# Kernel tuning notes

Hardware: AMD Instinct MI355X
Metric: run time of the kernel (lower is better)

The kernel has to match this reference:

```python
import jax, jax.numpy as jnp
import numpy as np

NUM_INTERVALS = 12
DOMAIN_MIN = -10.0
DOMAIN_MAX = 0.0


def _build_pla_coeffs(num_intervals=NUM_INTERVALS, dmin=DOMAIN_MIN, dmax=DOMAIN_MAX):
    """Least-squares linear fit of exp(x) on each interval (matches np.polyfit in source)."""
    xs = np.linspace(dmin, dmax, 1001)
    ys = np.exp(xs)
    edges = np.linspace(dmin, dmax, num_intervals + 1)
    ms, cs = [], []
    for i in range(num_intervals):
        mask = (xs >= edges[i]) & (xs <= edges[i + 1])
        m, c = np.polyfit(xs[mask], ys[mask], 1)
        ms.append(m)
        cs.append(c)
    # 'intervals' buffer in source stores only the LOWER edge of each interval (len = num_intervals)
    return (np.asarray(ms, np.float32), np.asarray(cs, np.float32), edges[:num_intervals].astype(np.float32))


def setup_inputs() -> dict:
    key = jax.random.key(0)
    scores = jax.random.normal(key, (8, 12, 512, 512), dtype=jnp.float32)
    m_np, c_np, a_np = _build_pla_coeffs()
    return {
        "scores": scores,
        "coeffs_m": jnp.asarray(m_np),
        "coeffs_c": jnp.asarray(c_np),
        "intervals": jnp.asarray(a_np),
    }


def reference(scores, coeffs_m, coeffs_c, intervals):
    # 1) stable shift by row max
    max_scores = jnp.max(scores, axis=-1, keepdims=True)
    shifted = scores - max_scores

    # 2) snap to Q32.26 fixed point
    fp_scale = 2.0 ** 26
    fx = jnp.clip(jnp.round(shifted * fp_scale), -(2.0 ** 31), 2.0 ** 31 - 1) / fp_scale

    # 3) piecewise-linear exp: bucket search against interval lower edges + coeff gather
    xc = jnp.clip(fx, DOMAIN_MIN, DOMAIN_MAX)
    # sum(x >= a_i) == searchsorted(a, x, side='right'); original clamps idx to len(intervals)-2
    idx = jnp.clip(jnp.searchsorted(intervals, xc, side="right") - 1, 0, intervals.shape[0] - 2)
    exps = coeffs_m[idx] * xc + coeffs_c[idx]

    # 4) normalize
    softmax_out = exps / (jnp.sum(exps, axis=-1, keepdims=True) + 1e-9)

    # 5) per-tensor symmetric INT8 fake-quant (STE form; same forward value)
    qmax = 127.0
    scale = jnp.maximum(jnp.max(jnp.abs(softmax_out)) / qmax, 1e-8)
    q = jnp.clip(jnp.round(softmax_out / scale), -qmax, qmax) * scale
    return softmax_out + jax.lax.stop_gradient(q - softmax_out)
```

## Files before the change

kernel.cpp:

```cpp
#include <hip/hip_runtime.h>

#define THREADS 256
#define WPB 4
#define ROW_LEN 512
#define NB 2048

typedef float f4 __attribute__((ext_vector_type(4)));
typedef char  c8 __attribute__((ext_vector_type(8)));

__device__ __forceinline__ float wave_reduce_max(float v) {
#pragma unroll
    for (int o = 32; o > 0; o >>= 1) v = fmaxf(v, __shfl_xor(v, o));
    return v;
}
__device__ __forceinline__ float wave_reduce_sum(float v) {
#pragma unroll
    for (int o = 32; o > 0; o >>= 1) v += __shfl_xor(v, o);
    return v;
}

__global__ __launch_bounds__(THREADS) void pla_pass0(
    const float* __restrict__ scores,
    const float* __restrict__ coeffs_m,
    const float* __restrict__ coeffs_c,
    const float* __restrict__ intervals,
    char* __restrict__ svq,
    float* __restrict__ rowg,
    float* __restrict__ slots,
    int nrows)
{
    __shared__ float2 s_mc[12];
    __shared__ float  s_a[13];
    __shared__ float  s_bm[WPB];

    const int tid = threadIdx.x;
    if (tid < 12) {
        s_mc[tid] = make_float2(coeffs_m[tid], coeffs_c[tid]);
        s_a[tid]  = intervals[tid];
    }
    if (tid == 12) s_a[12] = __builtin_inff();
    __syncthreads();

    const int wave = tid >> 6;
    const int lane = tid & 63;

    const float c10 = coeffs_c[10];
    const float k0  = 127.0f / c10;

    const int ngroups = (nrows + WPB - 1) / WPB;
    float bmax = 0.0f;

    for (int g = blockIdx.x; g < ngroups; g += NB) {
        const int row = g * WPB + wave;
        if (row >= nrows) continue;

        const float4* rp = reinterpret_cast<const float4*>(scores + (size_t)row * ROW_LEN);
        float4 v0 = rp[lane];
        float4 v1 = rp[lane + 64];
        float x[8] = {v0.x, v0.y, v0.z, v0.w, v1.x, v1.y, v1.z, v1.w};

        float mx = fmaxf(fmaxf(fmaxf(x[0], x[1]), fmaxf(x[2], x[3])),
                         fmaxf(fmaxf(x[4], x[5]), fmaxf(x[6], x[7])));
        mx = wave_reduce_max(mx);

        float e[8];
        float sum = 0.0f;
#pragma unroll
        for (int j = 0; j < 8; ++j) {
            float sh = x[j] - mx;
            float t = rintf(sh * 67108864.0f);
            float fx = t * 1.4901161193847656e-8f;
            float xc = fmaxf(fx, -10.0f);

            int gi = (int)((xc + 10.0f) * 1.2f);
            gi = min(max(gi, 0), 11);
            if (xc < s_a[gi])            gi -= 1;
            else if (xc >= s_a[gi + 1])  gi += 1;
            int idx = min(gi, 10);

            float2 p = s_mc[idx];
            float ev = p.x * xc + p.y;
            e[j] = ev;
            sum += ev;
        }
        sum = wave_reduce_sum(sum);
        const float inv = 1.0f / (sum + 1e-9f);

        c8 q;
#pragma unroll
        for (int j = 0; j < 8; ++j) q[j] = (char)(int)rintf(e[j] * k0);
        reinterpret_cast<c8*>(svq + (size_t)row * ROW_LEN)[lane] = q;

        if (lane == 0) {
            rowg[row] = c10 * inv * (1.0f / 127.0f);
            bmax = fmaxf(bmax, c10 * inv);
        }
    }

    if (lane == 0) s_bm[wave] = bmax;
    __syncthreads();
    if (tid == 0) {
        float bm = fmaxf(fmaxf(s_bm[0], s_bm[1]), fmaxf(s_bm[2], s_bm[3]));
        slots[blockIdx.x] = bm;
    }
}

__global__ __launch_bounds__(THREADS) void pla_pass1(
    const char* __restrict__ svq,
    const float* __restrict__ rowg,
    const float* __restrict__ slots,
    float* __restrict__ out,
    int nrows)
{
    __shared__ float s_red[WPB];
    const int tid  = threadIdx.x;
    const int wave = tid >> 6;
    const int lane = tid & 63;

    float m = 0.0f;
    for (int i = tid; i < NB; i += THREADS) m = fmaxf(m, slots[i]);
    m = wave_reduce_max(m);
    if (lane == 0) s_red[wave] = m;
    __syncthreads();
    const float am = fmaxf(fmaxf(s_red[0], s_red[1]), fmaxf(s_red[2], s_red[3]));

    const float scale  = fmaxf(am * (1.0f / 127.0f), 1e-8f);
    const float iscale = 1.0f / scale;

    const int ngroups = (nrows + WPB - 1) / WPB;
    for (int g = blockIdx.x; g < ngroups; g += NB) {
        const int row = g * WPB + wave;
        if (row >= nrows) continue;

        const float f = rowg[row] * iscale;
        c8 a = reinterpret_cast<const c8*>(svq + (size_t)row * ROW_LEN)[lane];

        float o[8];
#pragma unroll
        for (int j = 0; j < 8; ++j) {
            float q = fminf(fmaxf(rintf((float)a[j] * f), -127.0f), 127.0f);
            o[j] = q * scale;
        }
        f4* op = reinterpret_cast<f4*>(out + (size_t)row * ROW_LEN);
        f4 w0 = {o[0], o[1], o[2], o[3]};
        f4 w1 = {o[4], o[5], o[6], o[7]};
        __builtin_nontemporal_store(w0, op + lane);
        __builtin_nontemporal_store(w1, op + lane + 64);
    }
}

extern "C" void kernel_launch(void* const* d_in, const int* in_sizes, int n_in,
                              void* d_out, int out_size, void* d_ws, size_t ws_size,
                              hipStream_t stream) {
    const float* scores    = (const float*)d_in[0];
    const float* coeffs_m  = (const float*)d_in[1];
    const float* coeffs_c  = (const float*)d_in[2];
    const float* intervals = (const float*)d_in[3];
    float* out = (float*)d_out;

    const int nrows = in_sizes[0] / ROW_LEN;

    float* slots = (float*)d_ws;
    float* rowg  = (float*)((char*)d_ws + (128 << 10));
    char*  svq   = (char*)d_ws + (1 << 20);

    pla_pass0<<<NB, THREADS, 0, stream>>>(
        scores, coeffs_m, coeffs_c, intervals, svq, rowg, slots, nrows);
    pla_pass1<<<NB, THREADS, 0, stream>>>(svq, rowg, slots, out, nrows);
}
```

Baseline: 52.30 us.

## Fuse two passes into one persistent kernel with a grid-wide atomic barrier

Merges the two kernels into a single launch. Each block keeps its quantized rows and per-row factors in shared memory, publishes its block max, then spins on striped atomic counters until every block has arrived, reads the global max and writes the output. This removes the int8 workspace round-trip through global memory and the second kernel launch. In exchange it adds a memset, a spin-wait barrier that needs all 2048 blocks to be co-resident (launch bounds raised to 8 blocks per CU to allow that), and a fast path that only applies when the row count matches the fixed shape.

```diff
diff --git a/kernel.cpp b/kernel.cpp
--- a/kernel.cpp
+++ b/kernel.cpp
@@ -4,6 +4,10 @@
 #define WPB 4
 #define ROW_LEN 512
 #define NB 2048
+#define FTRIPS 6
+#define NCNT 64
+#define CSTRIDE 32
+#define AGENT __HIP_MEMORY_SCOPE_AGENT
 
 typedef float f4 __attribute__((ext_vector_type(4)));
 typedef char  c8 __attribute__((ext_vector_type(8)));
@@ -18,20 +22,44 @@
     for (int o = 32; o > 0; o >>= 1) v += __shfl_xor(v, o);
     return v;
 }
-
-__global__ __launch_bounds__(THREADS) void pla_pass0(
+__device__ __forceinline__ unsigned wave_reduce_sum_u(unsigned v) {
+#pragma unroll
+    for (int o = 32; o > 0; o >>= 1) v += __shfl_xor(v, o);
+    return v;
+}
+
+__device__ __forceinline__ float pla_eval(float xv, float mx,
+                                          const float* s_a, const float2* s_mc) {
+    float sh = xv - mx;
+    float t  = rintf(sh * 67108864.0f);
+    float fx = t * 1.4901161193847656e-8f;
+    float xc = fmaxf(fx, -10.0f);
+    int gi = (int)fmaf(xc, 1.2f, 12.0f);
+    gi = min(gi, 11);
+    if (xc < s_a[gi])            gi -= 1;
+    else if (xc >= s_a[gi + 1])  gi += 1;
+    int idx = min(gi, 10);
+    float2 p = s_mc[idx];
+    return fmaf(p.x, xc, p.y);
+}
+
+#define MAX8(x) fmaxf(fmaxf(fmaxf(x[0], x[1]), fmaxf(x[2], x[3])), \
+                      fmaxf(fmaxf(x[4], x[5]), fmaxf(x[6], x[7])))
+
+__global__ __launch_bounds__(THREADS, 8) void pla_fused(
     const float* __restrict__ scores,
     const float* __restrict__ coeffs_m,
     const float* __restrict__ coeffs_c,
     const float* __restrict__ intervals,
-    char* __restrict__ svq,
-    float* __restrict__ rowg,
-    float* __restrict__ slots,
-    int nrows)
+    float* __restrict__ bslots,
+    unsigned* __restrict__ counts,
+    float* __restrict__ out)
 {
     __shared__ float2 s_mc[12];
     __shared__ float  s_a[13];
     __shared__ float  s_bm[WPB];
+    __shared__ c8     s_q[WPB][FTRIPS][64];
+    __shared__ float  s_f[WPB][FTRIPS];
 
     const int tid = threadIdx.x;
     if (tid < 12) {
@@ -43,79 +71,152 @@
 
     const int wave = tid >> 6;
     const int lane = tid & 63;
-
     const float c10 = coeffs_c[10];
     const float k0  = 127.0f / c10;
 
+    float bmax = 0.0f;
+
+#pragma unroll
+    for (int t = 0; t < FTRIPS; ++t) {
+        const int row = (blockIdx.x + t * NB) * WPB + wave;
+        const f4* rp = reinterpret_cast<const f4*>(scores + (size_t)row * ROW_LEN);
+        f4 v0 = rp[lane];
+        f4 v1 = rp[lane + 64];
+        float x[8] = {v0.x, v0.y, v0.z, v0.w, v1.x, v1.y, v1.z, v1.w};
+
+        float mx = MAX8(x);
+        mx = wave_reduce_max(mx);
+
+        float sum = 0.0f;
+        c8 q;
+#pragma unroll
+        for (int j = 0; j < 8; ++j) {
+            float ev = pla_eval(x[j], mx, s_a, s_mc);
+            sum += ev;
+            q[j] = (char)(int)rintf(ev * k0);
+        }
+        s_q[wave][t][lane] = q;
+
+        sum = wave_reduce_sum(sum);
+        const float inv = 1.0f / (sum + 1e-9f);
+        if (lane == 0) {
+            s_f[wave][t] = c10 * inv * (1.0f / 127.0f);
+            bmax = fmaxf(bmax, c10 * inv);
+        }
+    }
+    if (lane == 0) s_bm[wave] = bmax;
+    __syncthreads();
+
+    if (tid == 0) {
+        float bm = fmaxf(fmaxf(s_bm[0], s_bm[1]), fmaxf(s_bm[2], s_bm[3]));
+        __hip_atomic_store(&bslots[blockIdx.x], bm, __ATOMIC_RELAXED, AGENT);
+        __hip_atomic_fetch_add(&counts[(blockIdx.x & (NCNT - 1)) * CSTRIDE],
+                               1u, __ATOMIC_RELEASE, AGENT);
+    }
+
+    if (tid < 64) {
+        unsigned total;
+        do {
+            __builtin_amdgcn_s_sleep(16);
+            unsigned c = __hip_atomic_load(&counts[tid * CSTRIDE],
+                                           __ATOMIC_RELAXED, AGENT);
+            total = wave_reduce_sum_u(c);
+        } while (total < (unsigned)NB);
+    }
+    __syncthreads();
+    __builtin_amdgcn_fence(__ATOMIC_ACQUIRE, "agent");
+
+    float m = 0.0f;
+    for (int i = tid; i < NB; i += THREADS)
+        m = fmaxf(m, __hip_atomic_load(&bslots[i], __ATOMIC_RELAXED, AGENT));
+    m = wave_reduce_max(m);
+    if (lane == 0) s_bm[wave] = m;
+    __syncthreads();
+    const float am = fmaxf(fmaxf(s_bm[0], s_bm[1]), fmaxf(s_bm[2], s_bm[3]));
+
+    const float scale  = fmaxf(am * (1.0f / 127.0f), 1e-8f);
+    const float iscale = 1.0f / scale;
+
+#pragma unroll
+    for (int t = 0; t < FTRIPS; ++t) {
+        const int row = (blockIdx.x + t * NB) * WPB + wave;
+        const float f = s_f[wave][t] * iscale;
+        c8 a = s_q[wave][t][lane];
+
+        float o[8];
+#pragma unroll
+        for (int j = 0; j < 8; ++j) {
+            float q = fminf(fmaxf(rintf((float)a[j] * f), -127.0f), 127.0f);
+            o[j] = q * scale;
+        }
+        f4* op = reinterpret_cast<f4*>(out + (size_t)row * ROW_LEN);
+        f4 w0 = {o[0], o[1], o[2], o[3]};
+        f4 w1 = {o[4], o[5], o[6], o[7]};
+        __builtin_nontemporal_store(w0, op + lane);
+        __builtin_nontemporal_store(w1, op + lane + 64);
+    }
+}
+
+__global__ __launch_bounds__(THREADS) void pla_pass0_gen(
+    const float* __restrict__ scores,
+    const float* __restrict__ coeffs_m,
+    const float* __restrict__ coeffs_c,
+    const float* __restrict__ intervals,
+    char* __restrict__ svq, float* __restrict__ rowg,
+    float* __restrict__ slots, int nrows)
+{
+    __shared__ float2 s_mc[12];
+    __shared__ float  s_a[13];
+    __shared__ float  s_bm[WPB];
+
+    const int tid = threadIdx.x;
+    if (tid < 12) {
+        s_mc[tid] = make_float2(coeffs_m[tid], coeffs_c[tid]);
+        s_a[tid]  = intervals[tid];
+    }
+    if (tid == 12) s_a[12] = __builtin_inff();
+    __syncthreads();
+
+    const int wave = tid >> 6, lane = tid & 63;
+    const float c10 = coeffs_c[10], k0 = 127.0f / c10;
+    float bmax = 0.0f;
+
     const int ngroups = (nrows + WPB - 1) / WPB;
-    float bmax = 0.0f;
-
     for (int g = blockIdx.x; g < ngroups; g += NB) {
         const int row = g * WPB + wave;
         if (row >= nrows) continue;
-
-        const float4* rp = reinterpret_cast<const float4*>(scores + (size_t)row * ROW_LEN);
-        float4 v0 = rp[lane];
-        float4 v1 = rp[lane + 64];
+        const f4* rp = reinterpret_cast<const f4*>(scores + (size_t)row * ROW_LEN);
+        f4 v0 = rp[lane], v1 = rp[lane + 64];
         float x[8] = {v0.x, v0.y, v0.z, v0.w, v1.x, v1.y, v1.z, v1.w};
-
-        float mx = fmaxf(fmaxf(fmaxf(x[0], x[1]), fmaxf(x[2], x[3])),
-                         fmaxf(fmaxf(x[4], x[5]), fmaxf(x[6], x[7])));
+        float mx = MAX8(x);
         mx = wave_reduce_max(mx);
-
-        float e[8];
-        float sum = 0.0f;
-#pragma unroll
-        for (int j = 0; j < 8; ++j) {
-            float sh = x[j] - mx;
-            float t = rintf(sh * 67108864.0f);
-            float fx = t * 1.4901161193847656e-8f;
-            float xc = fmaxf(fx, -10.0f);
-
-            int gi = (int)((xc + 10.0f) * 1.2f);
-            gi = min(max(gi, 0), 11);
-            if (xc < s_a[gi])            gi -= 1;
-            else if (xc >= s_a[gi + 1])  gi += 1;
-            int idx = min(gi, 10);
-
-            float2 p = s_mc[idx];
-            float ev = p.x * xc + p.y;
-            e[j] = ev;
+        float sum = 0.0f; c8 q;
+#pragma unroll
+        for (int j = 0; j < 8; ++j) {
+            float ev = pla_eval(x[j], mx, s_a, s_mc);
             sum += ev;
-        }
+            q[j] = (char)(int)rintf(ev * k0);
+        }
+        reinterpret_cast<c8*>(svq + (size_t)row * ROW_LEN)[lane] = q;
         sum = wave_reduce_sum(sum);
         const float inv = 1.0f / (sum + 1e-9f);
-
-        c8 q;
-#pragma unroll
-        for (int j = 0; j < 8; ++j) q[j] = (char)(int)rintf(e[j] * k0);
-        reinterpret_cast<c8*>(svq + (size_t)row * ROW_LEN)[lane] = q;
-
         if (lane == 0) {
             rowg[row] = c10 * inv * (1.0f / 127.0f);
             bmax = fmaxf(bmax, c10 * inv);
         }
     }
-
     if (lane == 0) s_bm[wave] = bmax;
     __syncthreads();
-    if (tid == 0) {
-        float bm = fmaxf(fmaxf(s_bm[0], s_bm[1]), fmaxf(s_bm[2], s_bm[3]));
-        slots[blockIdx.x] = bm;
-    }
-}
-
-__global__ __launch_bounds__(THREADS) void pla_pass1(
-    const char* __restrict__ svq,
-    const float* __restrict__ rowg,
-    const float* __restrict__ slots,
-    float* __restrict__ out,
-    int nrows)
+    if (tid == 0)
+        slots[blockIdx.x] = fmaxf(fmaxf(s_bm[0], s_bm[1]), fmaxf(s_bm[2], s_bm[3]));
+}
+
+__global__ __launch_bounds__(THREADS) void pla_pass1_gen(
+    const char* __restrict__ svq, const float* __restrict__ rowg,
+    const float* __restrict__ slots, float* __restrict__ out, int nrows)
 {
     __shared__ float s_red[WPB];
-    const int tid  = threadIdx.x;
-    const int wave = tid >> 6;
-    const int lane = tid & 63;
+    const int tid = threadIdx.x, wave = tid >> 6, lane = tid & 63;
 
     float m = 0.0f;
     for (int i = tid; i < NB; i += THREADS) m = fmaxf(m, slots[i]);
@@ -123,7 +224,6 @@
     if (lane == 0) s_red[wave] = m;
     __syncthreads();
     const float am = fmaxf(fmaxf(s_red[0], s_red[1]), fmaxf(s_red[2], s_red[3]));
-
     const float scale  = fmaxf(am * (1.0f / 127.0f), 1e-8f);
     const float iscale = 1.0f / scale;
 
@@ -131,10 +231,8 @@
     for (int g = blockIdx.x; g < ngroups; g += NB) {
         const int row = g * WPB + wave;
         if (row >= nrows) continue;
-
         const float f = rowg[row] * iscale;
         c8 a = reinterpret_cast<const c8*>(svq + (size_t)row * ROW_LEN)[lane];
-
         float o[8];
 #pragma unroll
         for (int j = 0; j < 8; ++j) {
@@ -160,11 +258,18 @@
 
     const int nrows = in_sizes[0] / ROW_LEN;
 
-    float* slots = (float*)d_ws;
-    float* rowg  = (float*)((char*)d_ws + (128 << 10));
-    char*  svq   = (char*)d_ws + (1 << 20);
-
-    pla_pass0<<<NB, THREADS, 0, stream>>>(
-        scores, coeffs_m, coeffs_c, intervals, svq, rowg, slots, nrows);
-    pla_pass1<<<NB, THREADS, 0, stream>>>(svq, rowg, slots, out, nrows);
-}
+    unsigned* counts = (unsigned*)d_ws;
+    float*    bslots = (float*)((char*)d_ws + (64 << 10));
+    float*    rowg   = (float*)((char*)d_ws + (128 << 10));
+    char*     svq    = (char*)d_ws + (1 << 20);
+
+    if (nrows == NB * WPB * FTRIPS) {
+        hipMemsetAsync(d_ws, 0, NCNT * CSTRIDE * sizeof(unsigned), stream);
+        pla_fused<<<NB, THREADS, 0, stream>>>(
+            scores, coeffs_m, coeffs_c, intervals, bslots, counts, out);
+    } else {
+        pla_pass0_gen<<<NB, THREADS, 0, stream>>>(
+            scores, coeffs_m, coeffs_c, intervals, svq, rowg, bslots, nrows);
+        pla_pass1_gen<<<NB, THREADS, 0, stream>>>(svq, rowg, bslots, out, nrows);
+    }
+}
```

Result: slower. 161.1 us (+208.0%).
